# Kernel optimization log

Measured on AMD Instinct MI355X. Metric: run time of the kernel, lower is better.

## Reference

```python
import jax, jax.numpy as jnp
import numpy as np

EMBED_DIM = 1024
NUM_HEADS = 16
HEAD_DIM = EMBED_DIM // NUM_HEADS


def setup_inputs() -> dict:
    key = jax.random.key(0)
    k_x, k_wqkv, k_bqkv, k_wp, k_bp = jax.random.split(key, 5)
    B, N, C = 4, 2048, EMBED_DIM
    bound_qkv = 1.0 / np.sqrt(C)
    bound_p = 1.0 / np.sqrt(C)
    return {
        "x": jax.random.normal(k_x, (B, N, C), dtype=jnp.float32),
        # nn.Linear stores weight as [out, in]; we keep that layout and use x @ W.T
        "w_qkv": jax.random.uniform(k_wqkv, (3 * C, C), jnp.float32, -bound_qkv, bound_qkv),
        "b_qkv": jax.random.uniform(k_bqkv, (3 * C,), jnp.float32, -bound_qkv, bound_qkv),
        "w_proj": jax.random.uniform(k_wp, (C, C), jnp.float32, -bound_p, bound_p),
        "b_proj": jax.random.uniform(k_bp, (C,), jnp.float32, -bound_p, bound_p),
    }


def reference(x, w_qkv, b_qkv, w_proj, b_proj):
    B, N, C = x.shape
    H, D = NUM_HEADS, HEAD_DIM
    qkv = x @ w_qkv.T + b_qkv                      # [B, N, 3C]
    qkv = qkv.reshape(B, N, 3, H, D)
    q = qkv[:, :, 0].transpose(0, 2, 1, 3)          # [B, H, N, D]
    k = qkv[:, :, 1].transpose(0, 2, 1, 3)
    v = qkv[:, :, 2].transpose(0, 2, 1, 3)
    scale = jnp.asarray(D, x.dtype) ** -0.5
    attn = jnp.einsum('bhqd,bhkd->bhqk', q, k) * scale  # [B, H, N, N]
    attn = jax.nn.softmax(attn, axis=-1)
    out = jnp.einsum('bhqk,bhkd->bhqd', attn, v)        # [B, H, N, D]
    out = out.transpose(0, 2, 1, 3).reshape(B, N, C)
    return out @ w_proj.T + b_proj
```

## Files before the change

### kernel.cpp

```cpp
#include <hip/hip_runtime.h>

typedef unsigned short u16;
typedef __attribute__((ext_vector_type(8))) short short8;
typedef __attribute__((ext_vector_type(4))) short s16x4;
typedef __attribute__((ext_vector_type(8))) _Float16 half8;
typedef __attribute__((ext_vector_type(4))) float f32x4;
typedef __attribute__((ext_vector_type(16))) float f32x16;
typedef __attribute__((ext_vector_type(4))) unsigned int u32x4;

#define DEVI static __device__ __forceinline__

static constexpr int B_ = 4, N_ = 2048, C_ = 1024, H_ = 16, D_ = 64;
static constexpr int M_ = B_ * N_;
static constexpr int C3 = 3072;

DEVI u16 f2h(float f) {
  _Float16 h = (_Float16)f;
  return __builtin_bit_cast(u16, h);
}

DEVI unsigned pk2h(float lo, float hi) {
  return __builtin_bit_cast(unsigned, __builtin_amdgcn_cvt_pkrtz(lo, hi));
}

DEVI void gload_lds16(const void* g, void* lds) {
  __builtin_amdgcn_global_load_lds(
      (const __attribute__((address_space(1))) unsigned int*)g,
      (__attribute__((address_space(3))) unsigned int*)lds, 16, 0, 0);
}

__global__ __launch_bounds__(256) void f32_to_f16_all(const float* __restrict__ x,
                                                      const float* __restrict__ wq,
                                                      const float* __restrict__ wp,
                                                      u16* __restrict__ x16,
                                                      u16* __restrict__ wq16,
                                                      u16* __restrict__ wp16) {
  int idx = blockIdx.x * 256 + threadIdx.x;
  const float* s;
  u16* d;
  int base;
  if (idx < 1048576) {
    s = x; d = x16; base = idx;
  } else if (idx < 1048576 + 393216) {
    s = wq; d = wq16; base = idx - 1048576;
  } else {
    s = wp; d = wp16; base = idx - 1441792;
  }
  const float* sp = s + (size_t)base * 8;
  f32x4 f0 = *(const f32x4*)sp;
  f32x4 f1 = *(const f32x4*)(sp + 4);
  short8 o;
#pragma unroll
  for (int j = 0; j < 8; ++j) o[j] = (short)f2h(j < 4 ? f0[j] : f1[j - 4]);
  *(short8*)(d + (size_t)base * 8) = o;
}

__global__ __launch_bounds__(256) void gemm_qkv(const u16* __restrict__ A,
                                                const u16* __restrict__ Bm,
                                                const float* __restrict__ bias,
                                                u16* __restrict__ q16,
                                                u16* __restrict__ kf,
                                                u16* __restrict__ vf) {
  __shared__ u16 SH[128 * 136];
  u16* As = SH;
  u16* Bs = SH + 128 * 64;
  const int tid = threadIdx.x;
  const int w = tid >> 6, l = tid & 63;
  const int wr = w >> 1, wc = w & 1;
  const int l15 = l & 15, lg = l >> 4;
  const int e7 = l15 & 7;
  const int nx = gridDim.x;
  int bid = blockIdx.y * nx + blockIdx.x;
  int cpx = (nx * gridDim.y) >> 3;
  int swz = (bid & 7) * cpx + (bid >> 3);
  int bx = swz % nx, by = swz / nx;
  const u16* Ab = A + (size_t)(bx * 128) * C_;
  const u16* Bb = Bm + (size_t)(by * 128) * C_;
  const int srow = tid >> 3;
  const int sgc8 = (((tid & 7) ^ ((tid >> 3) & 7)) * 8);
  const int fc0 = (lg ^ e7) << 4;
  const int fc1 = ((4 + lg) ^ e7) << 4;
  f32x4 acc[4][4];
#pragma unroll
  for (int m = 0; m < 4; ++m)
#pragma unroll
    for (int n = 0; n < 4; ++n) acc[m][n] = (f32x4){0.f, 0.f, 0.f, 0.f};

  for (int kt = 0; kt < C_; kt += 64) {
    __syncthreads();
#pragma unroll
    for (int i = 0; i < 4; ++i) {
      int r = i * 32 + srow;
      gload_lds16(Ab + (size_t)r * C_ + kt + sgc8, (char*)As + i * 4096 + w * 1024);
      gload_lds16(Bb + (size_t)r * C_ + kt + sgc8, (char*)Bs + i * 4096 + w * 1024);
    }
    __syncthreads();
#pragma unroll
    for (int kk = 0; kk < 2; ++kk) {
      const int fco = kk ? fc1 : fc0;
      half8 af[4], bf[4];
#pragma unroll
      for (int m = 0; m < 4; ++m)
        af[m] = __builtin_bit_cast(half8, *(const short8*)((const char*)As +
                    (wr * 64 + m * 16 + l15) * 128 + fco));
#pragma unroll
      for (int n = 0; n < 4; ++n)
        bf[n] = __builtin_bit_cast(half8, *(const short8*)((const char*)Bs +
                    (wc * 64 + n * 16 + l15) * 128 + fco));
#pragma unroll
      for (int m = 0; m < 4; ++m)
#pragma unroll
        for (int n = 0; n < 4; ++n)
          acc[m][n] = __builtin_amdgcn_mfma_f32_16x16x32_f16(af[m], bf[n], acc[m][n], 0, 0, 0);
    }
  }

  __syncthreads();
#pragma unroll
  for (int n = 0; n < 4; ++n) {
    int colL = wc * 64 + n * 16 + l15;
    float bval = bias[by * 128 + colL];
#pragma unroll
    for (int m = 0; m < 4; ++m)
#pragma unroll
      for (int i = 0; i < 4; ++i)
        SH[(wr * 64 + m * 16 + lg * 4 + i) * 136 + colL] = f2h(acc[m][n][i] + bval);
  }
  __syncthreads();

  if (by < 8) {
    const int c8 = l & 15;
    const int rb = w * 32 + (l >> 4);
    u16* qb = q16 + (size_t)(bx * 128) * C_ + by * 128;
#pragma unroll
    for (int j = 0; j < 8; ++j) {
      int r = rb + j * 4;
      *(short8*)(qb + (size_t)r * C_ + c8 * 8) = *(const short8*)&SH[r * 136 + c8 * 8];
    }
  } else if (by < 16) {
    const int h_loc = w & 1, t_loc = w >> 1;
    const int l31k = l & 31, hi2 = l >> 5;
    const int bh = (bx >> 4) * 16 + (by - 8) * 2 + h_loc;
    const int t = (bx & 15) * 2 + t_loc;
    u16* kb = kf + (size_t)(bh * 32 + t) * 4096;
#pragma unroll
    for (int j = 0; j < 8; ++j) {
      int kh = j >> 2, df = j & 3;
      int keyL = t_loc * 64 + kh * 32 + l31k;
      int colL = h_loc * 64 + (df * 2 + hi2) * 8;
      *(short8*)(kb + (j * 64 + l) * 8) = *(const short8*)&SH[keyL * 136 + colL];
    }
  } else {
    const int h_loc = w & 1, t_loc = w >> 1;
    const int l31v = l & 31, hi2 = l >> 5;
    const int bh = (bx >> 4) * 16 + (by - 16) * 2 + h_loc;
    const int t = (bx & 15) * 2 + t_loc;
    u16* vb = vf + (size_t)(bh * 32 + t) * 4096;
#pragma unroll
    for (int j = 0; j < 8; ++j) {
      int vh = j >> 2, kc = j & 3;
      int colL = h_loc * 64 + vh * 32 + l31v;
      short8 o;
#pragma unroll
      for (int jj = 0; jj < 8; ++jj) {
        int keyL = t_loc * 64 + kc * 16 + (jj & 3) + 8 * (jj >> 2) + 4 * hi2;
        o[jj] = (short)SH[keyL * 136 + colL];
      }
      *(short8*)(vb + (j * 64 + l) * 8) = o;
    }
  }
}

__global__ __launch_bounds__(256) void gemm_bt(const u16* __restrict__ A,
                                               const u16* __restrict__ Bm,
                                               const float* __restrict__ bias,
                                               float* __restrict__ outp, int Nout) {
  __shared__ u16 As[128 * 64];
  __shared__ u16 Bs[128 * 64];
  const int tid = threadIdx.x;
  const int w = tid >> 6, l = tid & 63;
  const int wr = w >> 1, wc = w & 1;
  const int l15 = l & 15, lg = l >> 4;
  const int e7 = l15 & 7;
  const int nx = gridDim.x;
  int bid = blockIdx.y * nx + blockIdx.x;
  int cpx = (nx * gridDim.y) >> 3;
  int swz = (bid & 7) * cpx + (bid >> 3);
  int bx = swz % nx, by = swz / nx;
  const u16* Ab = A + (size_t)(bx * 128) * C_;
  const u16* Bb = Bm + (size_t)(by * 128) * C_;
  const int srow = tid >> 3;
  const int sgc8 = (((tid & 7) ^ ((tid >> 3) & 7)) * 8);
  const int fc0 = (lg ^ e7) << 4;
  const int fc1 = ((4 + lg) ^ e7) << 4;
  f32x4 acc[4][4];
#pragma unroll
  for (int m = 0; m < 4; ++m)
#pragma unroll
    for (int n = 0; n < 4; ++n) acc[m][n] = (f32x4){0.f, 0.f, 0.f, 0.f};

  for (int kt = 0; kt < C_; kt += 64) {
    __syncthreads();
#pragma unroll
    for (int i = 0; i < 4; ++i) {
      int r = i * 32 + srow;
      gload_lds16(Ab + (size_t)r * C_ + kt + sgc8, (char*)As + i * 4096 + w * 1024);
      gload_lds16(Bb + (size_t)r * C_ + kt + sgc8, (char*)Bs + i * 4096 + w * 1024);
    }
    __syncthreads();
#pragma unroll
    for (int kk = 0; kk < 2; ++kk) {
      const int fco = kk ? fc1 : fc0;
      half8 af[4], bf[4];
#pragma unroll
      for (int m = 0; m < 4; ++m)
        af[m] = __builtin_bit_cast(half8, *(const short8*)((const char*)As +
                    (wr * 64 + m * 16 + l15) * 128 + fco));
#pragma unroll
      for (int n = 0; n < 4; ++n)
        bf[n] = __builtin_bit_cast(half8, *(const short8*)((const char*)Bs +
                    (wc * 64 + n * 16 + l15) * 128 + fco));
#pragma unroll
      for (int m = 0; m < 4; ++m)
#pragma unroll
        for (int n = 0; n < 4; ++n)
          acc[m][n] = __builtin_amdgcn_mfma_f32_16x16x32_f16(af[m], bf[n], acc[m][n], 0, 0, 0);
    }
  }
#pragma unroll
  for (int m = 0; m < 4; ++m)
#pragma unroll
    for (int n = 0; n < 4; ++n) {
      int col = by * 128 + wc * 64 + n * 16 + l15;
      float bval = bias[col];
#pragma unroll
      for (int i = 0; i < 4; ++i) {
        int row = bx * 128 + wr * 64 + m * 16 + lg * 4 + i;
        outp[(size_t)row * Nout + col] = acc[m][n][i] + bval;
      }
    }
}

__global__ __launch_bounds__(256, 2) void attn_fused(const u16* __restrict__ q16,
                                                     const u16* __restrict__ kf,
                                                     const u16* __restrict__ vf,
                                                     u16* __restrict__ att) {
  const int tid = threadIdx.x;
  const int w = tid >> 6, l = tid & 63;
  const int l31 = l & 31, hi = l >> 5;
  int bid = blockIdx.y * gridDim.x + blockIdx.x;
  int swz = (bid & 7) * 64 + (bid >> 3);
  const int qt = swz & 7, bh = swz >> 3;
  const int b = bh >> 4, h = bh & 15;
  const int qb = qt * 256 + w * 64;

  const float sc2 = 0.125f * 1.4426950408889634f;
  half8 qfA[4], qfB[4];
  {
    const _Float16 sch = (_Float16)sc2;
    const u16* qrowA = q16 + (size_t)(b * N_ + qb + l31) * C_ + h * D_ + hi * 8;
    const u16* qrowB = qrowA + (size_t)32 * C_;
#pragma unroll
    for (int df = 0; df < 4; ++df) {
      half8 qa = __builtin_bit_cast(half8, *(const short8*)(qrowA + df * 16));
      half8 qc = __builtin_bit_cast(half8, *(const short8*)(qrowB + df * 16));
#pragma unroll
      for (int j = 0; j < 8; ++j) { qa[j] *= sch; qc[j] *= sch; }
      qfA[df] = qa;
      qfB[df] = qc;
    }
  }

  f32x16 aA0, aA1, aB0, aB1;
#pragma unroll
  for (int j = 0; j < 16; ++j) { aA0[j] = 0.f; aA1[j] = 0.f; aB0[j] = 0.f; aB1[j] = 0.f; }
  float lrowA = 0.f, lrowB = 0.f;

  const u16* kp = kf + (size_t)bh * 32 * 4096;
  const u16* vp = vf + (size_t)bh * 32 * 4096;
  const int loff = l * 8;

#define MKPF(SV, J0, OUT)                                                      \
  {                                                                            \
    u32x4 wq = {pk2h(SV[J0 + 0], SV[J0 + 1]), pk2h(SV[J0 + 2], SV[J0 + 3]),   \
                pk2h(SV[J0 + 4], SV[J0 + 5]), pk2h(SV[J0 + 6], SV[J0 + 7])};   \
    OUT = __builtin_bit_cast(half8, wq);                                       \
  }

  for (int t = 0; t < 32; ++t) {
    const u16* kt = kp + t * 4096;
    const u16* vt = vp + t * 4096;

    half8 kfr[2][4];
#pragma unroll
    for (int kh = 0; kh < 2; ++kh)
#pragma unroll
      for (int df = 0; df < 4; ++df)
        kfr[kh][df] = __builtin_bit_cast(half8,
            *(const short8*)(kt + ((kh * 4 + df) * 64) * 8 + loff));

    f32x16 sA0, sA1;
#pragma unroll
    for (int j = 0; j < 16; ++j) { sA0[j] = 0.f; sA1[j] = 0.f; }
    __builtin_amdgcn_s_setprio(1);
#pragma unroll
    for (int df = 0; df < 4; ++df) {
      sA0 = __builtin_amdgcn_mfma_f32_32x32x16_f16(kfr[0][df], qfA[df], sA0, 0, 0, 0);
      sA1 = __builtin_amdgcn_mfma_f32_32x32x16_f16(kfr[1][df], qfA[df], sA1, 0, 0, 0);
    }
    __builtin_amdgcn_s_setprio(0);
    float suA[4] = {0.f, 0.f, 0.f, 0.f};
#pragma unroll
    for (int j = 0; j < 16; ++j) {
      sA0[j] = __builtin_amdgcn_exp2f(sA0[j]);
      suA[j & 3] += sA0[j];
    }
#pragma unroll
    for (int j = 0; j < 16; ++j) {
      sA1[j] = __builtin_amdgcn_exp2f(sA1[j]);
      suA[j & 3] += sA1[j];
    }
    lrowA += (suA[0] + suA[1]) + (suA[2] + suA[3]);
    half8 pfA0, pfA1, pfA2, pfA3;
    MKPF(sA0, 0, pfA0)
    MKPF(sA0, 8, pfA1)
    MKPF(sA1, 0, pfA2)
    MKPF(sA1, 8, pfA3)

    f32x16 sB0, sB1;
#pragma unroll
    for (int j = 0; j < 16; ++j) { sB0[j] = 0.f; sB1[j] = 0.f; }
    __builtin_amdgcn_s_setprio(1);
#pragma unroll
    for (int df = 0; df < 4; ++df) {
      sB0 = __builtin_amdgcn_mfma_f32_32x32x16_f16(kfr[0][df], qfB[df], sB0, 0, 0, 0);
      sB1 = __builtin_amdgcn_mfma_f32_32x32x16_f16(kfr[1][df], qfB[df], sB1, 0, 0, 0);
    }
    __builtin_amdgcn_s_setprio(0);

    half8 vfr[2][4];
#pragma unroll
    for (int vh = 0; vh < 2; ++vh)
#pragma unroll
      for (int kc = 0; kc < 4; ++kc)
        vfr[vh][kc] = __builtin_bit_cast(half8,
            *(const short8*)(vt + ((vh * 4 + kc) * 64) * 8 + loff));

    float suB[4] = {0.f, 0.f, 0.f, 0.f};
#pragma unroll
    for (int j = 0; j < 16; ++j) {
      sB0[j] = __builtin_amdgcn_exp2f(sB0[j]);
      suB[j & 3] += sB0[j];
    }
#pragma unroll
    for (int j = 0; j < 16; ++j) {
      sB1[j] = __builtin_amdgcn_exp2f(sB1[j]);
      suB[j & 3] += sB1[j];
    }
    lrowB += (suB[0] + suB[1]) + (suB[2] + suB[3]);
    half8 pfB0, pfB1, pfB2, pfB3;
    MKPF(sB0, 0, pfB0)
    MKPF(sB0, 8, pfB1)
    MKPF(sB1, 0, pfB2)
    MKPF(sB1, 8, pfB3)

    __builtin_amdgcn_s_setprio(1);
    aA0 = __builtin_amdgcn_mfma_f32_32x32x16_f16(vfr[0][0], pfA0, aA0, 0, 0, 0);
    aA1 = __builtin_amdgcn_mfma_f32_32x32x16_f16(vfr[1][0], pfA0, aA1, 0, 0, 0);
    aB0 = __builtin_amdgcn_mfma_f32_32x32x16_f16(vfr[0][0], pfB0, aB0, 0, 0, 0);
    aB1 = __builtin_amdgcn_mfma_f32_32x32x16_f16(vfr[1][0], pfB0, aB1, 0, 0, 0);
    aA0 = __builtin_amdgcn_mfma_f32_32x32x16_f16(vfr[0][1], pfA1, aA0, 0, 0, 0);
    aA1 = __builtin_amdgcn_mfma_f32_32x32x16_f16(vfr[1][1], pfA1, aA1, 0, 0, 0);
    aB0 = __builtin_amdgcn_mfma_f32_32x32x16_f16(vfr[0][1], pfB1, aB0, 0, 0, 0);
    aB1 = __builtin_amdgcn_mfma_f32_32x32x16_f16(vfr[1][1], pfB1, aB1, 0, 0, 0);
    aA0 = __builtin_amdgcn_mfma_f32_32x32x16_f16(vfr[0][2], pfA2, aA0, 0, 0, 0);
    aA1 = __builtin_amdgcn_mfma_f32_32x32x16_f16(vfr[1][2], pfA2, aA1, 0, 0, 0);
    aB0 = __builtin_amdgcn_mfma_f32_32x32x16_f16(vfr[0][2], pfB2, aB0, 0, 0, 0);
    aB1 = __builtin_amdgcn_mfma_f32_32x32x16_f16(vfr[1][2], pfB2, aB1, 0, 0, 0);
    aA0 = __builtin_amdgcn_mfma_f32_32x32x16_f16(vfr[0][3], pfA3, aA0, 0, 0, 0);
    aA1 = __builtin_amdgcn_mfma_f32_32x32x16_f16(vfr[1][3], pfA3, aA1, 0, 0, 0);
    aB0 = __builtin_amdgcn_mfma_f32_32x32x16_f16(vfr[0][3], pfB3, aB0, 0, 0, 0);
    aB1 = __builtin_amdgcn_mfma_f32_32x32x16_f16(vfr[1][3], pfB3, aB1, 0, 0, 0);
    __builtin_amdgcn_s_setprio(0);
  }
#undef MKPF

  {
    lrowA += __shfl_xor(lrowA, 32);
    lrowB += __shfl_xor(lrowB, 32);
    float rinvA = 1.0f / lrowA;
    float rinvB = 1.0f / lrowB;
    u16* orowA = att + (size_t)(b * N_ + qb + l31) * C_ + h * D_;
    u16* orowB = orowA + (size_t)32 * C_;
#pragma unroll
    for (int dt = 0; dt < 2; ++dt) {
#pragma unroll
      for (int r2 = 0; r2 < 4; ++r2) {
        int d0 = dt * 32 + r2 * 8 + hi * 4;
        s16x4 hvA, hvB;
#pragma unroll
        for (int i = 0; i < 4; ++i) {
          float vA = (dt ? aA1[r2 * 4 + i] : aA0[r2 * 4 + i]) * rinvA;
          float vB = (dt ? aB1[r2 * 4 + i] : aB0[r2 * 4 + i]) * rinvB;
          hvA[i] = (short)f2h(vA);
          hvB[i] = (short)f2h(vB);
        }
        *(s16x4*)(orowA + d0) = hvA;
        *(s16x4*)(orowB + d0) = hvB;
      }
    }
  }
}

extern "C" void kernel_launch(void* const* d_in, const int* in_sizes, int n_in,
                              void* d_out, int out_size, void* d_ws, size_t ws_size,
                              hipStream_t stream) {
  const float* x = (const float*)d_in[0];
  const float* w_qkv = (const float*)d_in[1];
  const float* b_qkv = (const float*)d_in[2];
  const float* w_proj = (const float*)d_in[3];
  const float* b_proj = (const float*)d_in[4];

  char* ws = (char*)d_ws;
  u16* q16  = (u16*)(ws + 0);
  u16* x16  = (u16*)(ws + 16777216);
  u16* wq16 = (u16*)(ws + 33554432);
  u16* wp16 = (u16*)(ws + 39845888);
  u16* kf   = (u16*)(ws + 41943040);
  u16* vf   = (u16*)(ws + 58720256);
  u16* att  = (u16*)(ws + 75497472);

  f32_to_f16_all<<<6144, 256, 0, stream>>>(x, w_qkv, w_proj, x16, wq16, wp16);

  gemm_qkv<<<dim3(64, 24), 256, 0, stream>>>(x16, wq16, b_qkv, q16, kf, vf);

  attn_fused<<<dim3(8, 64), 256, 0, stream>>>(q16, kf, vf, att);

  gemm_bt<<<dim3(64, 8), 256, 0, stream>>>(att, wp16, b_proj, (float*)d_out, C_);
}
```

Baseline: 186.7 us.

## Triple-buffer GEMM K-loop with async LDS loads and one barrier per step

```diff
diff --git a/kernel.cpp b/kernel.cpp
--- a/kernel.cpp
+++ b/kernel.cpp
@@ -61,14 +61,13 @@
                                                 u16* __restrict__ q16,
                                                 u16* __restrict__ kf,
                                                 u16* __restrict__ vf) {
-  __shared__ u16 SH[128 * 136];
-  u16* As = SH;
-  u16* Bs = SH + 128 * 64;
+  __shared__ u16 SH[24576];
+  u16* Asb = SH;
+  u16* Bsb = SH + 12288;
   const int tid = threadIdx.x;
   const int w = tid >> 6, l = tid & 63;
   const int wr = w >> 1, wc = w & 1;
   const int l15 = l & 15, lg = l >> 4;
-  const int e7 = l15 & 7;
   const int nx = gridDim.x;
   int bid = blockIdx.y * nx + blockIdx.x;
   int cpx = (nx * gridDim.y) >> 3;
@@ -76,42 +75,59 @@
   int bx = swz % nx, by = swz / nx;
   const u16* Ab = A + (size_t)(bx * 128) * C_;
   const u16* Bb = Bm + (size_t)(by * 128) * C_;
-  const int srow = tid >> 3;
-  const int sgc8 = (((tid & 7) ^ ((tid >> 3) & 7)) * 8);
-  const int fc0 = (lg ^ e7) << 4;
-  const int fc1 = ((4 + lg) ^ e7) << 4;
+  const int arow = tid >> 2;
+  const int ac8 = (((tid & 3) ^ ((tid >> 3) & 3)) * 8);
+  const int lgs = lg ^ ((l15 >> 1) & 3);
   f32x4 acc[4][4];
 #pragma unroll
   for (int m = 0; m < 4; ++m)
 #pragma unroll
     for (int n = 0; n < 4; ++n) acc[m][n] = (f32x4){0.f, 0.f, 0.f, 0.f};
 
-  for (int kt = 0; kt < C_; kt += 64) {
-    __syncthreads();
-#pragma unroll
-    for (int i = 0; i < 4; ++i) {
-      int r = i * 32 + srow;
-      gload_lds16(Ab + (size_t)r * C_ + kt + sgc8, (char*)As + i * 4096 + w * 1024);
-      gload_lds16(Bb + (size_t)r * C_ + kt + sgc8, (char*)Bs + i * 4096 + w * 1024);
-    }
-    __syncthreads();
-#pragma unroll
-    for (int kk = 0; kk < 2; ++kk) {
-      const int fco = kk ? fc1 : fc0;
-      half8 af[4], bf[4];
-#pragma unroll
-      for (int m = 0; m < 4; ++m)
-        af[m] = __builtin_bit_cast(half8, *(const short8*)((const char*)As +
-                    (wr * 64 + m * 16 + l15) * 128 + fco));
+  auto STAGE = [&](int t, int bb) {
+    const int kt = t * 32;
+#pragma unroll
+    for (int i = 0; i < 2; ++i) {
+      gload_lds16(Ab + (size_t)(i * 64 + arow) * C_ + kt + ac8,
+                  (char*)Asb + bb * 8192 + (i * 64 + w * 16) * 64);
+      gload_lds16(Bb + (size_t)(i * 64 + arow) * C_ + kt + ac8,
+                  (char*)Bsb + bb * 8192 + (i * 64 + w * 16) * 64);
+    }
+  };
+
+  STAGE(0, 0);
+  STAGE(1, 1);
+  asm volatile("s_waitcnt vmcnt(4)" ::: "memory");
+  __builtin_amdgcn_sched_barrier(0);
+  __builtin_amdgcn_s_barrier();
+  __builtin_amdgcn_sched_barrier(0);
+
+  for (int t = 0; t < 32; ++t) {
+    if (t + 2 < 32) STAGE(t + 2, (t + 2) % 3);
+    const char* Ap = (const char*)Asb + (t % 3) * 8192;
+    const char* Bp = (const char*)Bsb + (t % 3) * 8192;
+    half8 af[4], bf[4];
+#pragma unroll
+    for (int m = 0; m < 4; ++m)
+      af[m] = __builtin_bit_cast(half8, *(const short8*)(Ap +
+                  (wr * 64 + m * 16 + l15) * 64 + lgs * 16));
+#pragma unroll
+    for (int n = 0; n < 4; ++n)
+      bf[n] = __builtin_bit_cast(half8, *(const short8*)(Bp +
+                  (wc * 64 + n * 16 + l15) * 64 + lgs * 16));
+#pragma unroll
+    for (int m = 0; m < 4; ++m)
 #pragma unroll
       for (int n = 0; n < 4; ++n)
-        bf[n] = __builtin_bit_cast(half8, *(const short8*)((const char*)Bs +
-                    (wc * 64 + n * 16 + l15) * 128 + fco));
-#pragma unroll
-      for (int m = 0; m < 4; ++m)
-#pragma unroll
-        for (int n = 0; n < 4; ++n)
-          acc[m][n] = __builtin_amdgcn_mfma_f32_16x16x32_f16(af[m], bf[n], acc[m][n], 0, 0, 0);
+        acc[m][n] = __builtin_amdgcn_mfma_f32_16x16x32_f16(af[m], bf[n], acc[m][n], 0, 0, 0);
+    if (t + 1 < 32) {
+      if (t + 2 < 32)
+        asm volatile("s_waitcnt vmcnt(4)" ::: "memory");
+      else
+        asm volatile("s_waitcnt vmcnt(0)" ::: "memory");
+      __builtin_amdgcn_sched_barrier(0);
+      __builtin_amdgcn_s_barrier();
+      __builtin_amdgcn_sched_barrier(0);
     }
   }
 
@@ -175,13 +191,12 @@
                                                const u16* __restrict__ Bm,
                                                const float* __restrict__ bias,
                                                float* __restrict__ outp, int Nout) {
-  __shared__ u16 As[128 * 64];
-  __shared__ u16 Bs[128 * 64];
+  __shared__ u16 As[3][128 * 32];
+  __shared__ u16 Bs[3][128 * 32];
   const int tid = threadIdx.x;
   const int w = tid >> 6, l = tid & 63;
   const int wr = w >> 1, wc = w & 1;
   const int l15 = l & 15, lg = l >> 4;
-  const int e7 = l15 & 7;
   const int nx = gridDim.x;
   int bid = blockIdx.y * nx + blockIdx.x;
   int cpx = (nx * gridDim.y) >> 3;
@@ -189,44 +204,62 @@
   int bx = swz % nx, by = swz / nx;
   const u16* Ab = A + (size_t)(bx * 128) * C_;
   const u16* Bb = Bm + (size_t)(by * 128) * C_;
-  const int srow = tid >> 3;
-  const int sgc8 = (((tid & 7) ^ ((tid >> 3) & 7)) * 8);
-  const int fc0 = (lg ^ e7) << 4;
-  const int fc1 = ((4 + lg) ^ e7) << 4;
+  const int arow = tid >> 2;
+  const int ac8 = (((tid & 3) ^ ((tid >> 3) & 3)) * 8);
+  const int lgs = lg ^ ((l15 >> 1) & 3);
   f32x4 acc[4][4];
 #pragma unroll
   for (int m = 0; m < 4; ++m)
 #pragma unroll
     for (int n = 0; n < 4; ++n) acc[m][n] = (f32x4){0.f, 0.f, 0.f, 0.f};
 
-  for (int kt = 0; kt < C_; kt += 64) {
-    __syncthreads();
-#pragma unroll
-    for (int i = 0; i < 4; ++i) {
-      int r = i * 32 + srow;
-      gload_lds16(Ab + (size_t)r * C_ + kt + sgc8, (char*)As + i * 4096 + w * 1024);
-      gload_lds16(Bb + (size_t)r * C_ + kt + sgc8, (char*)Bs + i * 4096 + w * 1024);
-    }
-    __syncthreads();
-#pragma unroll
-    for (int kk = 0; kk < 2; ++kk) {
-      const int fco = kk ? fc1 : fc0;
-      half8 af[4], bf[4];
-#pragma unroll
-      for (int m = 0; m < 4; ++m)
-        af[m] = __builtin_bit_cast(half8, *(const short8*)((const char*)As +
-                    (wr * 64 + m * 16 + l15) * 128 + fco));
+  auto STAGE = [&](int t, int bb) {
+    const int kt = t * 32;
+#pragma unroll
+    for (int i = 0; i < 2; ++i) {
+      gload_lds16(Ab + (size_t)(i * 64 + arow) * C_ + kt + ac8,
+                  (char*)As[bb] + (i * 64 + w * 16) * 64);
+      gload_lds16(Bb + (size_t)(i * 64 + arow) * C_ + kt + ac8,
+                  (char*)Bs[bb] + (i * 64 + w * 16) * 64);
+    }
+  };
+
+  STAGE(0, 0);
+  STAGE(1, 1);
+  asm volatile("s_waitcnt vmcnt(4)" ::: "memory");
+  __builtin_amdgcn_sched_barrier(0);
+  __builtin_amdgcn_s_barrier();
+  __builtin_amdgcn_sched_barrier(0);
+
+  for (int t = 0; t < 32; ++t) {
+    if (t + 2 < 32) STAGE(t + 2, (t + 2) % 3);
+    const char* Ap = (const char*)As[t % 3];
+    const char* Bp = (const char*)Bs[t % 3];
+    half8 af[4], bf[4];
+#pragma unroll
+    for (int m = 0; m < 4; ++m)
+      af[m] = __builtin_bit_cast(half8, *(const short8*)(Ap +
+                  (wr * 64 + m * 16 + l15) * 64 + lgs * 16));
+#pragma unroll
+    for (int n = 0; n < 4; ++n)
+      bf[n] = __builtin_bit_cast(half8, *(const short8*)(Bp +
+                  (wc * 64 + n * 16 + l15) * 64 + lgs * 16));
+#pragma unroll
+    for (int m = 0; m < 4; ++m)
 #pragma unroll
       for (int n = 0; n < 4; ++n)
-        bf[n] = __builtin_bit_cast(half8, *(const short8*)((const char*)Bs +
-                    (wc * 64 + n * 16 + l15) * 128 + fco));
-#pragma unroll
-      for (int m = 0; m < 4; ++m)
-#pragma unroll
-        for (int n = 0; n < 4; ++n)
-          acc[m][n] = __builtin_amdgcn_mfma_f32_16x16x32_f16(af[m], bf[n], acc[m][n], 0, 0, 0);
-    }
-  }
+        acc[m][n] = __builtin_amdgcn_mfma_f32_16x16x32_f16(af[m], bf[n], acc[m][n], 0, 0, 0);
+    if (t + 1 < 32) {
+      if (t + 2 < 32)
+        asm volatile("s_waitcnt vmcnt(4)" ::: "memory");
+      else
+        asm volatile("s_waitcnt vmcnt(0)" ::: "memory");
+      __builtin_amdgcn_sched_barrier(0);
+      __builtin_amdgcn_s_barrier();
+      __builtin_amdgcn_sched_barrier(0);
+    }
+  }
+
 #pragma unroll
   for (int m = 0; m < 4; ++m)
 #pragma unroll
```

After: 197.2 us. +5.7%, slower.
